# Kernel optimization log

Measured on AMD Instinct MI355X. Metric: run time of the kernel, lower is better.

Reference implementation:

```python
import jax, jax.numpy as jnp
import numpy as np

B, D_IN, H, N_LAYERS, D_OUT = 262144, 8, 128, 3, 1


def setup_inputs() -> dict:
    key = jax.random.key(0)
    ks = jax.random.split(key, 18)
    rn = lambda k, shape, fan: (jax.random.normal(k, shape, jnp.float32) / np.sqrt(fan))
    return {
        "x": jax.random.normal(ks[0], (B, D_IN), jnp.float32),
        "Sw_w": rn(ks[1], (D_IN, H), D_IN),
        "Sw_b": rn(ks[2], (H,), D_IN),
        "Uz": rn(ks[3], (N_LAYERS, D_IN, H), D_IN),
        "Wsz_w": rn(ks[4], (N_LAYERS, H, H), H),
        "Wsz_b": rn(ks[5], (N_LAYERS, H), H),
        "Ug": rn(ks[6], (N_LAYERS, D_IN, H), D_IN),
        "Wsg_w": rn(ks[7], (N_LAYERS, H, H), H),
        "Wsg_b": rn(ks[8], (N_LAYERS, H), H),
        "Ur": rn(ks[9], (N_LAYERS, D_IN, H), D_IN),
        "Wsr_w": rn(ks[10], (N_LAYERS, H, H), H),
        "Wsr_b": rn(ks[11], (N_LAYERS, H), H),
        "Uh": rn(ks[12], (N_LAYERS, D_IN, H), D_IN),
        "Wsh_w": rn(ks[13], (N_LAYERS, H, H), H),
        "Wsh_b": rn(ks[14], (N_LAYERS, H), H),
        "Wf_w": rn(ks[15], (H, D_OUT), H),
        "Wf_b": rn(ks[16], (D_OUT,), H),
    }


def reference(x, Sw_w, Sw_b, Uz, Wsz_w, Wsz_b, Ug, Wsg_w, Wsg_b,
              Ur, Wsr_w, Wsr_b, Uh, Wsh_w, Wsh_b, Wf_w, Wf_b):
    # x: [B, D_in]; S: [B, H]
    S = x @ Sw_w + Sw_b
    n = Uz.shape[0]
    for i in range(n):  # small fixed layer count
        S = jax.nn.sigmoid(S)
        Z = jax.nn.sigmoid(x @ Uz[i] + S @ Wsz_w[i] + Wsz_b[i])
        G = jax.nn.sigmoid(x @ Ug[i] + S @ Wsg_w[i] + Wsg_b[i])
        R = jax.nn.sigmoid(x @ Ur[i] + S @ Wsr_w[i] + Wsr_b[i])
        H_ = jnp.tanh(x @ Uh[i] + (S * R) @ Wsh_w[i] + Wsh_b[i])
        S = (1.0 - G) * H_ + Z * S
    return S @ Wf_w + Wf_b  # [B, D_out]
```

## Files before the change

kernel.cpp:

```cpp
#include <hip/hip_runtime.h>

typedef __bf16 bf16_t;
typedef __bf16 bf16x4 __attribute__((ext_vector_type(4)));
typedef __bf16 bf16x8 __attribute__((ext_vector_type(8)));
typedef float f32x4 __attribute__((ext_vector_type(4)));

#define NL 3
#define HD 128
#define ROWS 64
#define STR 136
#define THREADS 512
#define BATCH 262144
#define NBLK (BATCH / ROWS)

#define SW_OFF 0
#define U_OFF  4096
#define W_OFF  53248
#define WS_ELEMS 249856

#define MFMA(a, b, c) __builtin_amdgcn_mfma_f32_16x16x32_bf16((a), (b), (c), 0, 0, 0)

#define LOG2E 1.4426950408889634f
__device__ __forceinline__ float sigm(float v) {
    return __builtin_amdgcn_rcpf(1.f + __builtin_amdgcn_exp2f(-LOG2E * v));
}
__device__ __forceinline__ float sigmn(float v) {
    return __builtin_amdgcn_rcpf(1.f + __builtin_amdgcn_exp2f(LOG2E * v));
}
__device__ __forceinline__ float tanh_f(float v) {
    return 1.f - 2.f * __builtin_amdgcn_rcpf(__builtin_amdgcn_exp2f((2.f * LOG2E) * v) + 1.f);
}

__global__ void dgm_prep(const float* __restrict__ SwW,
                         const float* __restrict__ Uz, const float* __restrict__ Wz,
                         const float* __restrict__ Ug, const float* __restrict__ Wg,
                         const float* __restrict__ Ur, const float* __restrict__ Wr,
                         const float* __restrict__ Uh, const float* __restrict__ Wh,
                         bf16_t* __restrict__ ws) {
    int idx = blockIdx.x * 256 + threadIdx.x;
    if (idx >= WS_ELEMS) return;
    const float* Us[4] = {Uz, Ug, Ur, Uh};
    const float* Wm[4] = {Wz, Wg, Wr, Wh};
    if (idx < U_OFF) {
        int ct = idx >> 9, rem = idx & 511, lane = rem >> 3, j = rem & 7;
        int q = lane >> 4, mm = lane & 15;
        int k = q * 8 + j, n = ct * 16 + mm;
        ws[idx] = (k < 8) ? (bf16_t)SwW[k * HD + n] : (bf16_t)0.f;
    } else if (idx < W_OFF) {
        int t = idx - U_OFF;
        int lg = t >> 12, r2 = t & 4095;
        int l = lg >> 2, g = lg & 3;
        int ct = r2 >> 9, rem = r2 & 511, lane = rem >> 3, j = rem & 7;
        int q = lane >> 4, mm = lane & 15;
        int k = q * 8 + j, n = ct * 16 + mm;
        ws[idx] = (k < 8) ? (bf16_t)Us[g][(l * 8 + k) * HD + n] : (bf16_t)0.f;
    } else {
        int t = idx - W_OFF;
        int lg = t >> 14, r2 = t & 16383;
        int l = lg >> 2, g = lg & 3;
        int ct = r2 >> 11, kc = (r2 >> 9) & 3, rem = r2 & 511, lane = rem >> 3, j = rem & 7;
        int q = lane >> 4, mm = lane & 15;
        int k = kc * 32 + q * 8 + j, n = ct * 16 + mm;
        ws[idx] = (bf16_t)Wm[g][(l * HD + k) * HD + n];
    }
}

__global__ __launch_bounds__(THREADS, 4) void dgm_main(
    const float* __restrict__ x,
    const float* __restrict__ Swb,
    const float* __restrict__ Bz, const float* __restrict__ Bg,
    const float* __restrict__ Br, const float* __restrict__ Bh,
    const float* __restrict__ WfW, const float* __restrict__ WfB,
    const bf16_t* __restrict__ ws,
    float* __restrict__ out) {
    __shared__ __align__(16) bf16_t s_sig[2][ROWS * STR];
    __shared__ __align__(16) bf16_t s_r[ROWS * STR];
    __shared__ float red[ROWS];

    const int tid = threadIdx.x;
    const int lane = tid & 63;
    const int ct = tid >> 6;
    const int m = lane & 15, q = lane >> 4;
    const int rb = blockIdx.x * ROWS;
    const int f0 = ct * 16 + q * 4;
    const int fragoff = (ct * 64 + lane) * 8;
    const int wfragoff = (ct * 4) * 512 + lane * 8;

    if (tid < ROWS) red[tid] = 0.f;

    {
        int r = tid >> 3, j = tid & 7;
        bf16_t xv = (bf16_t)x[(size_t)(rb + r) * 8 + j];
        s_sig[0][r * STR + 128 + j] = xv;
        s_sig[1][r * STR + 128 + j] = xv;
        s_r[r * STR + 128 + j] = xv;
    }
    __syncthreads();

    bf16x4 svp[4];

    {
        const f32x4 swb4 = *(const f32x4*)&Swb[f0];
        bf16x8 fSw = *(const bf16x8*)(ws + SW_OFF + fragoff);
#pragma unroll
        for (int bt = 0; bt < 4; bt++) {
            bf16x8 b = *(const bf16x8*)(&s_sig[0][(bt * 16 + m) * STR + 128]);
            f32x4 acc = {0.f, 0.f, 0.f, 0.f};
            acc = MFMA(fSw, b, acc);
            bf16x4 pk;
#pragma unroll
            for (int i = 0; i < 4; i++) pk[i] = (bf16_t)sigm(acc[i] + swb4[i]);
            svp[bt] = pk;
            *(bf16x4*)(&s_sig[0][(bt * 16 + m) * STR + f0]) = pk;
        }
    }
    __syncthreads();

#pragma unroll 1
    for (int l = 0; l < NL; l++) {
        const int cur = l & 1, nxt = cur ^ 1;
        const bf16_t* wb = ws + W_OFF + (size_t)l * 4 * 16384;
        const bf16_t* ub = ws + U_OFF + (size_t)l * 4 * 4096;

        {
            bf16x8 fU = *(const bf16x8*)(ub + 2 * 4096 + fragoff);
            bf16x8 fW[4];
#pragma unroll
            for (int kc = 0; kc < 4; kc++)
                fW[kc] = *(const bf16x8*)(wb + 2 * 16384 + wfragoff + kc * 512);
            const f32x4 br4 = *(const f32x4*)&Br[l * HD + f0];
#pragma unroll
            for (int bt = 0; bt < 4; bt++) {
                const bf16_t* bbase = &s_sig[cur][(bt * 16 + m) * STR];
                f32x4 aR = {0.f, 0.f, 0.f, 0.f};
#pragma unroll
                for (int kc = 0; kc < 4; kc++) {
                    bf16x8 b = *(const bf16x8*)(bbase + kc * 32 + q * 8);
                    aR = MFMA(fW[kc], b, aR);
                }
                {
                    bf16x8 b = *(const bf16x8*)(bbase + 128);
                    aR = MFMA(fU, b, aR);
                }
                bf16x4 pk;
#pragma unroll
                for (int i = 0; i < 4; i++)
                    pk[i] = (bf16_t)(sigm(aR[i] + br4[i]) * (float)svp[bt][i]);
                *(bf16x4*)(&s_r[(bt * 16 + m) * STR + f0]) = pk;
            }
        }
        __syncthreads();

        bf16x4 t1p[4];
        bf16x4 ogp[4];

        {
            bf16x8 fUz = *(const bf16x8*)(ub + 0 * 4096 + fragoff);
            bf16x8 fUg = *(const bf16x8*)(ub + 1 * 4096 + fragoff);
            bf16x8 fWz[4], fWg[4];
#pragma unroll
            for (int kc = 0; kc < 4; kc++) {
                fWz[kc] = *(const bf16x8*)(wb + 0 * 16384 + wfragoff + kc * 512);
                fWg[kc] = *(const bf16x8*)(wb + 1 * 16384 + wfragoff + kc * 512);
            }
            const f32x4 bz4 = *(const f32x4*)&Bz[l * HD + f0];
            const f32x4 bg4 = *(const f32x4*)&Bg[l * HD + f0];
#pragma unroll
            for (int bt = 0; bt < 4; bt++) {
                const bf16_t* bbase = &s_sig[cur][(bt * 16 + m) * STR];
                f32x4 aZ = {0.f, 0.f, 0.f, 0.f}, aG = {0.f, 0.f, 0.f, 0.f};
#pragma unroll
                for (int kc = 0; kc < 4; kc++) {
                    bf16x8 b = *(const bf16x8*)(bbase + kc * 32 + q * 8);
                    aZ = MFMA(fWz[kc], b, aZ);
                    aG = MFMA(fWg[kc], b, aG);
                }
                {
                    bf16x8 b = *(const bf16x8*)(bbase + 128);
                    aZ = MFMA(fUz, b, aZ);
                    aG = MFMA(fUg, b, aG);
                }
                bf16x4 t1, og;
#pragma unroll
                for (int i = 0; i < 4; i++) {
                    t1[i] = (bf16_t)(sigm(aZ[i] + bz4[i]) * (float)svp[bt][i]);
                    og[i] = (bf16_t)sigmn(aG[i] + bg4[i]);
                }
                t1p[bt] = t1;
                ogp[bt] = og;
            }
        }

        {
            bf16x8 fU = *(const bf16x8*)(ub + 3 * 4096 + fragoff);
            bf16x8 fW[4];
#pragma unroll
            for (int kc = 0; kc < 4; kc++)
                fW[kc] = *(const bf16x8*)(wb + 3 * 16384 + wfragoff + kc * 512);
            const f32x4 bh4 = *(const f32x4*)&Bh[l * HD + f0];
            const bool last = (l == NL - 1);
            const f32x4 wf4 = *(const f32x4*)&WfW[f0];
#pragma unroll
            for (int bt = 0; bt < 4; bt++) {
                const bf16_t* bbase = &s_r[(bt * 16 + m) * STR];
                f32x4 aH = {0.f, 0.f, 0.f, 0.f};
#pragma unroll
                for (int kc = 0; kc < 4; kc++) {
                    bf16x8 b = *(const bf16x8*)(bbase + kc * 32 + q * 8);
                    aH = MFMA(fW[kc], b, aH);
                }
                {
                    bf16x8 b = *(const bf16x8*)(bbase + 128);
                    aH = MFMA(fU, b, aH);
                }
                if (last) {
                    float p = 0.f;
#pragma unroll
                    for (int i = 0; i < 4; i++) {
                        float hh = tanh_f(aH[i] + bh4[i]);
                        float sn = (float)ogp[bt][i] * hh + (float)t1p[bt][i];
                        p += sn * wf4[i];
                    }
                    p += __shfl_xor(p, 16);
                    p += __shfl_xor(p, 32);
                    if (q == 0) atomicAdd(&red[bt * 16 + m], p);
                } else {
                    bf16x4 pk;
#pragma unroll
                    for (int i = 0; i < 4; i++) {
                        float hh = tanh_f(aH[i] + bh4[i]);
                        float sn = (float)ogp[bt][i] * hh + (float)t1p[bt][i];
                        pk[i] = (bf16_t)sigm(sn);
                    }
                    svp[bt] = pk;
                    *(bf16x4*)(&s_sig[nxt][(bt * 16 + m) * STR + f0]) = pk;
                }
            }
        }
        __syncthreads();
    }

    if (tid < ROWS) out[rb + tid] = red[tid] + WfB[0];
}

extern "C" void kernel_launch(void* const* d_in, const int* in_sizes, int n_in,
                              void* d_out, int out_size, void* d_ws, size_t ws_size,
                              hipStream_t stream) {
    const float* x   = (const float*)d_in[0];
    const float* SwW = (const float*)d_in[1];
    const float* Swb = (const float*)d_in[2];
    const float* Uz  = (const float*)d_in[3];
    const float* Wz  = (const float*)d_in[4];
    const float* Bz  = (const float*)d_in[5];
    const float* Ug  = (const float*)d_in[6];
    const float* Wg  = (const float*)d_in[7];
    const float* Bg  = (const float*)d_in[8];
    const float* Ur  = (const float*)d_in[9];
    const float* Wr  = (const float*)d_in[10];
    const float* Br  = (const float*)d_in[11];
    const float* Uh  = (const float*)d_in[12];
    const float* Wh  = (const float*)d_in[13];
    const float* Bh  = (const float*)d_in[14];
    const float* WfW = (const float*)d_in[15];
    const float* WfB = (const float*)d_in[16];
    bf16_t* ws = (bf16_t*)d_ws;
    float* out = (float*)d_out;

    if (ws_size < (size_t)WS_ELEMS * sizeof(bf16_t)) return;

    dgm_prep<<<(WS_ELEMS + 255) / 256, 256, 0, stream>>>(SwW, Uz, Wz, Ug, Wg, Ur, Wr, Uh, Wh, ws);
    dgm_main<<<NBLK, THREADS, 0, stream>>>(x, Swb, Bz, Bg, Br, Bh, WfW, WfB, ws, out);
}
```

Baseline: 287.3 us.

## Fold gate biases into U fragments via ones column and split Z/G passes

Folds the Sw, Z, G and R biases into the padded K slot of the U input fragments, and adds a constant-one column to the x region of the state buffer so the MFMA adds the bias. It also splits the fused Z/G pass into two passes to lower register pressure, and raises launch bounds from 4 to 6 waves. The reduction scratch is reused from padding in the state buffer. The aim is fewer bias loads and adds and higher occupancy, at the cost of a wider LDS stride and possibly more LDS reads and lost ILP from the split.

```diff
diff --git a/kernel.cpp b/kernel.cpp
--- a/kernel.cpp
+++ b/kernel.cpp
@@ -8,7 +8,8 @@
 #define NL 3
 #define HD 128
 #define ROWS 64
-#define STR 136
+#define SSTR 144
+#define RSTR 136
 #define THREADS 512
 #define BATCH 262144
 #define NBLK (BATCH / ROWS)
@@ -31,10 +32,10 @@
     return 1.f - 2.f * __builtin_amdgcn_rcpf(__builtin_amdgcn_exp2f((2.f * LOG2E) * v) + 1.f);
 }
 
-__global__ void dgm_prep(const float* __restrict__ SwW,
-                         const float* __restrict__ Uz, const float* __restrict__ Wz,
-                         const float* __restrict__ Ug, const float* __restrict__ Wg,
-                         const float* __restrict__ Ur, const float* __restrict__ Wr,
+__global__ void dgm_prep(const float* __restrict__ SwW, const float* __restrict__ Swb,
+                         const float* __restrict__ Uz, const float* __restrict__ Wz, const float* __restrict__ Bz,
+                         const float* __restrict__ Ug, const float* __restrict__ Wg, const float* __restrict__ Bg,
+                         const float* __restrict__ Ur, const float* __restrict__ Wr, const float* __restrict__ Br,
                          const float* __restrict__ Uh, const float* __restrict__ Wh,
                          bf16_t* __restrict__ ws) {
     int idx = blockIdx.x * 256 + threadIdx.x;
@@ -45,7 +46,8 @@
         int ct = idx >> 9, rem = idx & 511, lane = rem >> 3, j = rem & 7;
         int q = lane >> 4, mm = lane & 15;
         int k = q * 8 + j, n = ct * 16 + mm;
-        ws[idx] = (k < 8) ? (bf16_t)SwW[k * HD + n] : (bf16_t)0.f;
+        ws[idx] = (k < 8) ? (bf16_t)SwW[k * HD + n]
+                : (k == 8) ? (bf16_t)Swb[n] : (bf16_t)0.f;
     } else if (idx < W_OFF) {
         int t = idx - U_OFF;
         int lg = t >> 12, r2 = t & 4095;
@@ -53,7 +55,9 @@
         int ct = r2 >> 9, rem = r2 & 511, lane = rem >> 3, j = rem & 7;
         int q = lane >> 4, mm = lane & 15;
         int k = q * 8 + j, n = ct * 16 + mm;
-        ws[idx] = (k < 8) ? (bf16_t)Us[g][(l * 8 + k) * HD + n] : (bf16_t)0.f;
+        const float* Bs = (g == 0) ? Bz : (g == 1) ? Bg : (g == 2) ? Br : (const float*)0;
+        ws[idx] = (k < 8) ? (bf16_t)Us[g][(l * 8 + k) * HD + n]
+                : (k == 8 && g < 3) ? (bf16_t)Bs[l * HD + n] : (bf16_t)0.f;
     } else {
         int t = idx - W_OFF;
         int lg = t >> 14, r2 = t & 16383;
@@ -65,7 +69,7 @@
     }
 }
 
-__global__ __launch_bounds__(THREADS, 4) void dgm_main(
+__global__ __launch_bounds__(THREADS, 6) void dgm_main(
     const float* __restrict__ x,
     const float* __restrict__ Swb,
     const float* __restrict__ Bz, const float* __restrict__ Bg,
@@ -73,9 +77,8 @@
     const float* __restrict__ WfW, const float* __restrict__ WfB,
     const bf16_t* __restrict__ ws,
     float* __restrict__ out) {
-    __shared__ __align__(16) bf16_t s_sig[2][ROWS * STR];
-    __shared__ __align__(16) bf16_t s_r[ROWS * STR];
-    __shared__ float red[ROWS];
+    __shared__ __align__(16) bf16_t s_sig[2][ROWS * SSTR];
+    __shared__ __align__(16) bf16_t s_r[ROWS * RSTR];
 
     const int tid = threadIdx.x;
     const int lane = tid & 63;
@@ -85,33 +88,34 @@
     const int f0 = ct * 16 + q * 4;
     const int fragoff = (ct * 64 + lane) * 8;
     const int wfragoff = (ct * 4) * 512 + lane * 8;
-
-    if (tid < ROWS) red[tid] = 0.f;
+    const int xoff = 128 + (q ? 8 : 0);
 
     {
         int r = tid >> 3, j = tid & 7;
         bf16_t xv = (bf16_t)x[(size_t)(rb + r) * 8 + j];
-        s_sig[0][r * STR + 128 + j] = xv;
-        s_sig[1][r * STR + 128 + j] = xv;
-        s_r[r * STR + 128 + j] = xv;
+        s_sig[0][r * SSTR + 128 + j] = xv;
+        s_sig[1][r * SSTR + 128 + j] = xv;
+        s_r[r * RSTR + 128 + j] = xv;
+        bf16_t ov = (j == 0) ? (bf16_t)1.f : (bf16_t)0.f;
+        s_sig[0][r * SSTR + 136 + j] = ov;
+        s_sig[1][r * SSTR + 136 + j] = ov;
     }
     __syncthreads();
 
     bf16x4 svp[4];
 
     {
-        const f32x4 swb4 = *(const f32x4*)&Swb[f0];
         bf16x8 fSw = *(const bf16x8*)(ws + SW_OFF + fragoff);
 #pragma unroll
         for (int bt = 0; bt < 4; bt++) {
-            bf16x8 b = *(const bf16x8*)(&s_sig[0][(bt * 16 + m) * STR + 128]);
+            bf16x8 b = *(const bf16x8*)(&s_sig[0][(bt * 16 + m) * SSTR + xoff]);
             f32x4 acc = {0.f, 0.f, 0.f, 0.f};
             acc = MFMA(fSw, b, acc);
             bf16x4 pk;
 #pragma unroll
-            for (int i = 0; i < 4; i++) pk[i] = (bf16_t)sigm(acc[i] + swb4[i]);
+            for (int i = 0; i < 4; i++) pk[i] = (bf16_t)sigm(acc[i]);
             svp[bt] = pk;
-            *(bf16x4*)(&s_sig[0][(bt * 16 + m) * STR + f0]) = pk;
+            *(bf16x4*)(&s_sig[0][(bt * 16 + m) * SSTR + f0]) = pk;
         }
     }
     __syncthreads();
@@ -119,19 +123,21 @@
 #pragma unroll 1
     for (int l = 0; l < NL; l++) {
         const int cur = l & 1, nxt = cur ^ 1;
+        const bool last = (l == NL - 1);
         const bf16_t* wb = ws + W_OFF + (size_t)l * 4 * 16384;
         const bf16_t* ub = ws + U_OFF + (size_t)l * 4 * 4096;
 
+        if (last && tid < ROWS) *(float*)&s_sig[1][tid * SSTR + 138] = 0.f;
+
         {
             bf16x8 fU = *(const bf16x8*)(ub + 2 * 4096 + fragoff);
             bf16x8 fW[4];
 #pragma unroll
             for (int kc = 0; kc < 4; kc++)
                 fW[kc] = *(const bf16x8*)(wb + 2 * 16384 + wfragoff + kc * 512);
-            const f32x4 br4 = *(const f32x4*)&Br[l * HD + f0];
-#pragma unroll
-            for (int bt = 0; bt < 4; bt++) {
-                const bf16_t* bbase = &s_sig[cur][(bt * 16 + m) * STR];
+#pragma unroll
+            for (int bt = 0; bt < 4; bt++) {
+                const bf16_t* bbase = &s_sig[cur][(bt * 16 + m) * SSTR];
                 f32x4 aR = {0.f, 0.f, 0.f, 0.f};
 #pragma unroll
                 for (int kc = 0; kc < 4; kc++) {
@@ -139,14 +145,14 @@
                     aR = MFMA(fW[kc], b, aR);
                 }
                 {
-                    bf16x8 b = *(const bf16x8*)(bbase + 128);
+                    bf16x8 b = *(const bf16x8*)(bbase + xoff);
                     aR = MFMA(fU, b, aR);
                 }
                 bf16x4 pk;
 #pragma unroll
                 for (int i = 0; i < 4; i++)
-                    pk[i] = (bf16_t)(sigm(aR[i] + br4[i]) * (float)svp[bt][i]);
-                *(bf16x4*)(&s_r[(bt * 16 + m) * STR + f0]) = pk;
+                    pk[i] = (bf16_t)(sigm(aR[i]) * (float)svp[bt][i]);
+                *(bf16x4*)(&s_r[(bt * 16 + m) * RSTR + f0]) = pk;
             }
         }
         __syncthreads();
@@ -155,39 +161,56 @@
         bf16x4 ogp[4];
 
         {
-            bf16x8 fUz = *(const bf16x8*)(ub + 0 * 4096 + fragoff);
-            bf16x8 fUg = *(const bf16x8*)(ub + 1 * 4096 + fragoff);
-            bf16x8 fWz[4], fWg[4];
-#pragma unroll
-            for (int kc = 0; kc < 4; kc++) {
-                fWz[kc] = *(const bf16x8*)(wb + 0 * 16384 + wfragoff + kc * 512);
-                fWg[kc] = *(const bf16x8*)(wb + 1 * 16384 + wfragoff + kc * 512);
-            }
-            const f32x4 bz4 = *(const f32x4*)&Bz[l * HD + f0];
-            const f32x4 bg4 = *(const f32x4*)&Bg[l * HD + f0];
-#pragma unroll
-            for (int bt = 0; bt < 4; bt++) {
-                const bf16_t* bbase = &s_sig[cur][(bt * 16 + m) * STR];
-                f32x4 aZ = {0.f, 0.f, 0.f, 0.f}, aG = {0.f, 0.f, 0.f, 0.f};
-#pragma unroll
-                for (int kc = 0; kc < 4; kc++) {
-                    bf16x8 b = *(const bf16x8*)(bbase + kc * 32 + q * 8);
-                    aZ = MFMA(fWz[kc], b, aZ);
-                    aG = MFMA(fWg[kc], b, aG);
-                }
-                {
-                    bf16x8 b = *(const bf16x8*)(bbase + 128);
-                    aZ = MFMA(fUz, b, aZ);
-                    aG = MFMA(fUg, b, aG);
-                }
-                bf16x4 t1, og;
-#pragma unroll
-                for (int i = 0; i < 4; i++) {
-                    t1[i] = (bf16_t)(sigm(aZ[i] + bz4[i]) * (float)svp[bt][i]);
-                    og[i] = (bf16_t)sigmn(aG[i] + bg4[i]);
-                }
-                t1p[bt] = t1;
-                ogp[bt] = og;
+            bf16x8 fU = *(const bf16x8*)(ub + 0 * 4096 + fragoff);
+            bf16x8 fW[4];
+#pragma unroll
+            for (int kc = 0; kc < 4; kc++)
+                fW[kc] = *(const bf16x8*)(wb + 0 * 16384 + wfragoff + kc * 512);
+#pragma unroll
+            for (int bt = 0; bt < 4; bt++) {
+                const bf16_t* bbase = &s_sig[cur][(bt * 16 + m) * SSTR];
+                f32x4 aZ = {0.f, 0.f, 0.f, 0.f};
+#pragma unroll
+                for (int kc = 0; kc < 4; kc++) {
+                    bf16x8 b = *(const bf16x8*)(bbase + kc * 32 + q * 8);
+                    aZ = MFMA(fW[kc], b, aZ);
+                }
+                {
+                    bf16x8 b = *(const bf16x8*)(bbase + xoff);
+                    aZ = MFMA(fU, b, aZ);
+                }
+                bf16x4 pk;
+#pragma unroll
+                for (int i = 0; i < 4; i++)
+                    pk[i] = (bf16_t)(sigm(aZ[i]) * (float)svp[bt][i]);
+                t1p[bt] = pk;
+            }
+        }
+
+        {
+            bf16x8 fU = *(const bf16x8*)(ub + 1 * 4096 + fragoff);
+            bf16x8 fW[4];
+#pragma unroll
+            for (int kc = 0; kc < 4; kc++)
+                fW[kc] = *(const bf16x8*)(wb + 1 * 16384 + wfragoff + kc * 512);
+#pragma unroll
+            for (int bt = 0; bt < 4; bt++) {
+                const bf16_t* bbase = &s_sig[cur][(bt * 16 + m) * SSTR];
+                f32x4 aG = {0.f, 0.f, 0.f, 0.f};
+#pragma unroll
+                for (int kc = 0; kc < 4; kc++) {
+                    bf16x8 b = *(const bf16x8*)(bbase + kc * 32 + q * 8);
+                    aG = MFMA(fW[kc], b, aG);
+                }
+                {
+                    bf16x8 b = *(const bf16x8*)(bbase + xoff);
+                    aG = MFMA(fU, b, aG);
+                }
+                bf16x4 pk;
+#pragma unroll
+                for (int i = 0; i < 4; i++)
+                    pk[i] = (bf16_t)sigmn(aG[i]);
+                ogp[bt] = pk;
             }
         }
 
@@ -198,11 +221,10 @@
             for (int kc = 0; kc < 4; kc++)
                 fW[kc] = *(const bf16x8*)(wb + 3 * 16384 + wfragoff + kc * 512);
             const f32x4 bh4 = *(const f32x4*)&Bh[l * HD + f0];
-            const bool last = (l == NL - 1);
             const f32x4 wf4 = *(const f32x4*)&WfW[f0];
 #pragma unroll
             for (int bt = 0; bt < 4; bt++) {
-                const bf16_t* bbase = &s_r[(bt * 16 + m) * STR];
+                const bf16_t* bbase = &s_r[(bt * 16 + m) * RSTR];
                 f32x4 aH = {0.f, 0.f, 0.f, 0.f};
 #pragma unroll
                 for (int kc = 0; kc < 4; kc++) {
@@ -223,7 +245,8 @@
                     }
                     p += __shfl_xor(p, 16);
                     p += __shfl_xor(p, 32);
-                    if (q == 0) atomicAdd(&red[bt * 16 + m], p);
+                    if (q == 0)
+                        atomicAdd((float*)&s_sig[1][(bt * 16 + m) * SSTR + 138], p);
                 } else {
                     bf16x4 pk;
 #pragma unroll
@@ -233,14 +256,14 @@
                         pk[i] = (bf16_t)sigm(sn);
                     }
                     svp[bt] = pk;
-                    *(bf16x4*)(&s_sig[nxt][(bt * 16 + m) * STR + f0]) = pk;
+                    *(bf16x4*)(&s_sig[nxt][(bt * 16 + m) * SSTR + f0]) = pk;
                 }
             }
         }
         __syncthreads();
     }
 
-    if (tid < ROWS) out[rb + tid] = red[tid] + WfB[0];
+    if (tid < ROWS) out[rb + tid] = *(const float*)&s_sig[1][tid * SSTR + 138] + WfB[0];
 }
 
 extern "C" void kernel_launch(void* const* d_in, const int* in_sizes, int n_in,
@@ -268,6 +291,7 @@
 
     if (ws_size < (size_t)WS_ELEMS * sizeof(bf16_t)) return;
 
-    dgm_prep<<<(WS_ELEMS + 255) / 256, 256, 0, stream>>>(SwW, Uz, Wz, Ug, Wg, Ur, Wr, Uh, Wh, ws);
+    dgm_prep<<<(WS_ELEMS + 255) / 256, 256, 0, stream>>>(SwW, Swb, Uz, Wz, Bz, Ug, Wg, Bg,
+                                                         Ur, Wr, Br, Uh, Wh, ws);
     dgm_main<<<NBLK, THREADS, 0, stream>>>(x, Swb, Bz, Bg, Br, Bh, WfW, WfB, ws, out);
 }
```

Result: slower. 428.3 us (+49.1%).
